# Optimization experiments

Measured on AMD Instinct MI355X. Metric: run time of the kernel, lower is better.

The kernel has to match this reference:

```python
import jax, jax.numpy as jnp
import numpy as np

TEMP = 0.07
LN_EPS = 1e-5


def _l2norm(x, eps=1e-12):
    n = jnp.linalg.norm(x, axis=-1, keepdims=True)
    return x / jnp.maximum(n, eps)


def setup_inputs() -> dict:
    key = jax.random.key(0)
    ks = jax.random.split(key, 8)
    B, N, D, S = 1024, 100000, 1024, 2
    scale = 1.0 / np.sqrt(D)
    return {
        "q": jax.random.normal(ks[0], (B, D), jnp.float32),
        "bank_values": jax.random.normal(ks[1], (N, D), jnp.float32),
        "proj_w": jax.random.normal(ks[2], (S, D, D), jnp.float32) * scale,
        "proj_b": jax.random.normal(ks[3], (S, D), jnp.float32) * 0.01,
        "unify_w": jax.random.normal(ks[4], (S, D, D), jnp.float32) * scale,
        "unify_b": jax.random.normal(ks[5], (S, D), jnp.float32) * 0.01,
        "ln_gamma": jnp.ones((D,), jnp.float32),
        "ln_beta": jnp.zeros((D,), jnp.float32),
        "top_m": 32,
    }


def reference(q, bank_values, proj_w, proj_b, unify_w, unify_b, ln_gamma, ln_beta, top_m):
    # PrototypeBank.build: keys = L2-normalized values (detached)
    keys = _l2norm(bank_values)  # [N, D]
    num_scales = proj_w.shape[0]
    ref = jnp.zeros_like(q)
    for s in range(num_scales):  # small fixed structural loop
        p = q @ proj_w[s].T + proj_b[s]                       # [B, D] Linear
        scores = _l2norm(p) @ keys.T                          # [B, N] cosine
        top_s, top_i = jax.lax.top_k(scores, top_m)           # [B, m]
        attn = jax.nn.softmax(top_s / TEMP, axis=-1)          # [B, m]
        z = jnp.einsum('bm,bmd->bd', attn, bank_values[top_i])  # weighted gather-sum
        ref = ref + z @ unify_w[s].T + unify_b[s]
    mu = ref.mean(axis=-1, keepdims=True)
    var = ref.var(axis=-1, keepdims=True)
    out = (ref - mu) * jax.lax.rsqrt(var + LN_EPS) * ln_gamma + ln_beta
    return out
```

## Files before the change

### kernel.cpp

```cpp
#include <hip/hip_runtime.h>
#include <math.h>


static inline size_t align256(size_t x){ return (x + 255) & ~size_t(255); }

typedef short bf16x8 __attribute__((ext_vector_type(8)));
typedef float f32x4  __attribute__((ext_vector_type(4)));

#define GLOAD_LDS16(gp, lp) \
  __builtin_amdgcn_global_load_lds((const __attribute__((address_space(1))) unsigned int*)(gp), \
                                   (__attribute__((address_space(3))) unsigned int*)(lp), 16, 0, 0)

__device__ inline unsigned short f2bf(float f){
  unsigned int u = __float_as_uint(f);
  u += 0x7fffu + ((u >> 16) & 1u);
  return (unsigned short)(u >> 16);
}
__device__ inline float bf2f(unsigned int h16){
  return __uint_as_float(h16 << 16);
}

template<bool SCALE_OUT>
__global__ __launch_bounds__(256) void rnorm_convert_kernel(
    const float* __restrict__ X, float* __restrict__ rn,
    unsigned short* __restrict__ out, int rows, int D)
{
  int wv = threadIdx.x >> 6, lane = threadIdx.x & 63;
  int r = blockIdx.x * 4 + wv;
  if (r >= rows) return;
  const float4* xr = (const float4*)(X + (size_t)r * D);
  int nv = D >> 2;
  float ss = 0.f;
  for (int i = lane; i < nv; i += 64){
    float4 v = xr[i];
    ss = fmaf(v.x,v.x, fmaf(v.y,v.y, fmaf(v.z,v.z, fmaf(v.w,v.w, ss))));
  }
  #pragma unroll
  for (int off = 32; off; off >>= 1) ss += __shfl_xor(ss, off);
  float rinv = 1.f / fmaxf(sqrtf(ss), 1e-12f);
  if (lane == 0) rn[r] = rinv;
  const float sc = SCALE_OUT ? rinv : 1.f;
  unsigned short* orow = out + (size_t)r * D;
  for (int i = lane; i < (D >> 3); i += 64){
    float4 v0 = xr[i*2], v1 = xr[i*2+1];
    v0.x*=sc; v0.y*=sc; v0.z*=sc; v0.w*=sc;
    v1.x*=sc; v1.y*=sc; v1.z*=sc; v1.w*=sc;
    uint4 w;
    w.x = (unsigned)f2bf(v0.x) | ((unsigned)f2bf(v0.y) << 16);
    w.y = (unsigned)f2bf(v0.z) | ((unsigned)f2bf(v0.w) << 16);
    w.z = (unsigned)f2bf(v1.x) | ((unsigned)f2bf(v1.y) << 16);
    w.w = (unsigned)f2bf(v1.z) | ((unsigned)f2bf(v1.w) << 16);
    *(uint4*)(orow + i*8) = w;
  }
}

template<int RM, int RN, bool ACCUM>
__global__ __launch_bounds__(256) void gemm_nt_kernel(
    const float* __restrict__ A, const float* __restrict__ B,
    const float* __restrict__ bias, const float* __restrict__ bscale,
    float* __restrict__ C, int M, int Nn, int K, int Brows, int ldc)
{
  __shared__ float As[16][RM*64 + 4];
  __shared__ float Bs[16][RN*64 + 4];
  const int t  = threadIdx.x;
  const int tm = t >> 4, tn = t & 15;
  const int m0 = blockIdx.y * (RM*64), n0 = blockIdx.x * (RN*64);

  float acc[RM][RN][4][4];
  #pragma unroll
  for (int r=0;r<RM;++r)
    #pragma unroll
    for (int c=0;c<RN;++c)
      #pragma unroll
      for (int i=0;i<4;++i)
        #pragma unroll
        for (int j=0;j<4;++j) acc[r][c][i][j]=0.f;

  for (int kp = 0; kp < K; kp += 16){
    #pragma unroll
    for (int l = 0; l < RM; ++l){
      int li = t + l*256;
      int row = li >> 2, kq = (li & 3) << 2;
      float4 v = *(const float4*)(A + (size_t)(m0+row)*K + kp + kq);
      As[kq+0][row]=v.x; As[kq+1][row]=v.y; As[kq+2][row]=v.z; As[kq+3][row]=v.w;
    }
    #pragma unroll
    for (int l = 0; l < RN; ++l){
      int li = t + l*256;
      int row = li >> 2, kq = (li & 3) << 2;
      int gn = n0 + row;
      float4 v = make_float4(0.f,0.f,0.f,0.f);
      float sc = 1.f;
      if (gn < Brows){
        v = *(const float4*)(B + (size_t)gn*K + kp + kq);
        if (bscale) sc = bscale[gn];
      }
      Bs[kq+0][row]=v.x*sc; Bs[kq+1][row]=v.y*sc; Bs[kq+2][row]=v.z*sc; Bs[kq+3][row]=v.w*sc;
    }
    __syncthreads();
    #pragma unroll
    for (int kk = 0; kk < 16; ++kk){
      float av[RM][4], bv[RN][4];
      #pragma unroll
      for (int r=0;r<RM;++r){
        float4 a = *(const float4*)&As[kk][r*64 + tm*4];
        av[r][0]=a.x; av[r][1]=a.y; av[r][2]=a.z; av[r][3]=a.w;
      }
      #pragma unroll
      for (int c=0;c<RN;++c){
        float4 b = *(const float4*)&Bs[kk][c*64 + tn*4];
        bv[c][0]=b.x; bv[c][1]=b.y; bv[c][2]=b.z; bv[c][3]=b.w;
      }
      #pragma unroll
      for (int r=0;r<RM;++r)
        #pragma unroll
        for (int c=0;c<RN;++c)
          #pragma unroll
          for (int i=0;i<4;++i)
            #pragma unroll
            for (int j=0;j<4;++j)
              acc[r][c][i][j] = fmaf(av[r][i], bv[c][j], acc[r][c][i][j]);
    }
    __syncthreads();
  }

  #pragma unroll
  for (int r=0;r<RM;++r){
    #pragma unroll
    for (int i=0;i<4;++i){
      int gm = m0 + r*64 + tm*4 + i;
      #pragma unroll
      for (int c=0;c<RN;++c){
        int gn = n0 + c*64 + tn*4;
        if (gn >= Nn) continue;
        float* cp = C + (size_t)gm*ldc + gn;
        float o0=acc[r][c][i][0], o1=acc[r][c][i][1], o2=acc[r][c][i][2], o3=acc[r][c][i][3];
        if (gn + 3 < Nn){
          float4 o = make_float4(o0,o1,o2,o3);
          if (bias){ float4 bb = *(const float4*)&bias[gn]; o.x+=bb.x; o.y+=bb.y; o.z+=bb.z; o.w+=bb.w; }
          if (ACCUM){ float4 cc = *(const float4*)cp; o.x+=cc.x; o.y+=cc.y; o.z+=cc.z; o.w+=cc.w; }
          *(float4*)cp = o;
        } else {
          float ov[4] = {o0,o1,o2,o3};
          for (int j=0;j<4;++j){
            if (gn + j < Nn){
              float o = ov[j];
              if (bias)  o += bias[gn+j];
              if (ACCUM) o += cp[j];
              cp[j] = o;
            }
          }
        }
      }
    }
  }
}

__global__ __launch_bounds__(256) void scores_mfma_kernel(
    const unsigned short* __restrict__ Abf, const unsigned short* __restrict__ Bbf,
    unsigned short* __restrict__ C, int M, int Nn, int K, int ldc)
{
  __shared__ __align__(16) unsigned char smem[32768];

  const int t = threadIdx.x;
  const int lane = t & 63, wid = t >> 6;
  const int wm = wid >> 1, wn = wid & 1;
  const int l15 = lane & 15, l4 = lane >> 4;

  const int nwg = gridDim.x;
  const int q = nwg >> 3, r = nwg & 7;
  const int xcd = blockIdx.x & 7, idx = blockIdx.x >> 3;
  const int logical = (xcd < r ? xcd*(q+1) : r*(q+1) + (xcd-r)*q) + idx;
  const int mtiles = M >> 7;
  const int m0 = (logical % mtiles) * 128;
  const int n0 = (logical / mtiles) * 128;

  f32x4 acc[4][4];
  #pragma unroll
  for (int i=0;i<4;++i)
    #pragma unroll
    for (int j=0;j<4;++j) acc[i][j] = (f32x4)0.f;

  const int srow = t >> 3;
  const int sb   = (t & 7) * 16;
  const int ldsb = wid * 1024;

  for (int kp = 0; kp < K; kp += 64){
    #pragma unroll
    for (int i = 0; i < 4; ++i){
      int row = srow + i*32;
      int src = sb ^ ((row & 7) << 4);
      const unsigned char* ga = (const unsigned char*)Abf
          + ((size_t)(m0+row)*K + kp)*2 + src;
      GLOAD_LDS16(ga, smem + i*4096 + ldsb);
      int gn = n0 + row; if (gn >= Nn) gn = Nn - 1;
      const unsigned char* gb = (const unsigned char*)Bbf
          + ((size_t)gn*K + kp)*2 + src;
      GLOAD_LDS16(gb, smem + 16384 + i*4096 + ldsb);
    }
    __syncthreads();

    const unsigned char* As_ = smem;
    const unsigned char* Bs_ = smem + 16384;
    bf16x8 B0[4], B1[4];
    #pragma unroll
    for (int fn = 0; fn < 4; ++fn){
      int br = wn*64 + fn*16 + l15;
      int xr = (br & 7) << 4;
      const unsigned char* bp = Bs_ + br*128;
      B0[fn] = *(const bf16x8*)(bp + (( l4*16      ) ^ xr));
      B1[fn] = *(const bf16x8*)(bp + ((64 + l4*16 ) ^ xr));
    }
    #pragma unroll
    for (int fm = 0; fm < 4; ++fm){
      int ar = wm*64 + fm*16 + l15;
      int xr = (ar & 7) << 4;
      const unsigned char* ap = As_ + ar*128;
      bf16x8 A0 = *(const bf16x8*)(ap + (( l4*16      ) ^ xr));
      bf16x8 A1 = *(const bf16x8*)(ap + ((64 + l4*16 ) ^ xr));
      #pragma unroll
      for (int fn = 0; fn < 4; ++fn){
        acc[fm][fn] = __builtin_amdgcn_mfma_f32_16x16x32_bf16(A0, B0[fn], acc[fm][fn], 0,0,0);
        acc[fm][fn] = __builtin_amdgcn_mfma_f32_16x16x32_bf16(A1, B1[fn], acc[fm][fn], 0,0,0);
      }
    }
    __syncthreads();
  }

  #pragma unroll
  for (int fm = 0; fm < 4; ++fm){
    int row = m0 + wm*64 + fm*16 + l4*4;
    #pragma unroll
    for (int fn = 0; fn < 4; ++fn){
      int col = n0 + wn*64 + fn*16 + l15;
      if (col < Nn){
        unsigned short* cp = C + (size_t)row*ldc + col;
        #pragma unroll
        for (int r2 = 0; r2 < 4; ++r2) cp[(size_t)r2*ldc] = f2bf(acc[fm][fn][r2]);
      }
    }
  }
}

__global__ __launch_bounds__(256) void chunk_filter_kernel(
    const unsigned short* __restrict__ scores, int ldc, int colbase, int Nwindow,
    int NC, float* __restrict__ cand_s, int* __restrict__ cand_i,
    int chunk0, int nchunks_total, int cap, float eps)
{
  extern __shared__ float lds[];
  __shared__ float sv[256];
  __shared__ float tau_s;
  __shared__ int cnt;
  const int row = blockIdx.x, t = threadIdx.x;
  const int lc = blockIdx.y;
  const int col0l = lc * NC;
  int ncols = Nwindow - col0l; if (ncols > NC) ncols = NC;
  const int gchunk = chunk0 + lc;
  const unsigned short* sr = scores + (size_t)row * ldc + col0l;

  float m0 = -INFINITY, m1 = -INFINITY, m2 = -INFINITY, m3 = -INFINITY;
  const int nc8 = ncols >> 3;
  const uint4* sr8 = (const uint4*)sr;
  float4* lds4 = (float4*)lds;
  for (int j = t; j < nc8; j += 256){
    uint4 v = sr8[j];
    float4 a = make_float4(bf2f(v.x & 0xffffu), bf2f(v.x >> 16),
                           bf2f(v.y & 0xffffu), bf2f(v.y >> 16));
    float4 b = make_float4(bf2f(v.z & 0xffffu), bf2f(v.z >> 16),
                           bf2f(v.w & 0xffffu), bf2f(v.w >> 16));
    lds4[j*2]   = a;
    lds4[j*2+1] = b;
    m0 = fmaxf(m0, fmaxf(a.x, b.x)); m1 = fmaxf(m1, fmaxf(a.y, b.y));
    m2 = fmaxf(m2, fmaxf(a.z, b.z)); m3 = fmaxf(m3, fmaxf(a.w, b.w));
  }
  for (int j = (nc8 << 3) + t; j < ncols; j += 256){
    float v = bf2f((unsigned)sr[j]);
    lds[j] = v;
    m0 = fmaxf(m0, v);
  }
  sv[t] = fmaxf(fmaxf(m0, m1), fmaxf(m2, m3));
  __syncthreads();

  for (int k = 2; k <= 256; k <<= 1){
    for (int j = k >> 1; j > 0; j >>= 1){
      int p = t ^ j;
      float a = sv[t], b = sv[p];
      bool up = ((t & k) == 0);
      float keep = (t < p) ? (up ? fmaxf(a,b) : fminf(a,b))
                           : (up ? fminf(a,b) : fmaxf(a,b));
      __syncthreads();
      sv[t] = keep;
      __syncthreads();
    }
  }
  if (t == 0){ tau_s = sv[31]; cnt = 0; }
  __syncthreads();
  const float thr = tau_s - eps;

  float* cs = cand_s + ((size_t)row * nchunks_total + gchunk) * cap;
  int*   ci = cand_i + ((size_t)row * nchunks_total + gchunk) * cap;

  for (int j = t; j < ncols; j += 256){
    float v = lds[j];
    if (v >= thr){
      int pos = atomicAdd(&cnt, 1);
      if (pos < cap){ cs[pos] = v; ci[pos] = colbase + col0l + j; }
    }
  }
  __syncthreads();
  int n = cnt < cap ? cnt : cap;
  for (int j = n + t; j < cap; j += 256) ci[j] = -1;
}

__global__ __launch_bounds__(256) void select_softmax_gather_kernel(
    const float* __restrict__ cand_s, const int* __restrict__ cand_i,
    const float* __restrict__ p, const float* __restrict__ rn_bank,
    const float* __restrict__ pnorm, const float* __restrict__ bank,
    float* __restrict__ z, int ncap, int D, int topm, float invtemp, float eps)
{
  __shared__ float p_s[1024];
  __shared__ float vs[1024]; __shared__ int vi[1024];
  __shared__ float sv[256];
  __shared__ int   cidx[256];
  __shared__ float rv[256];
  __shared__ float tau_s;
  __shared__ int cnt;
  const int row = blockIdx.x, t = threadIdx.x;
  const int lane = t & 63, wid = t >> 6;

  const float4* pr = (const float4*)(p + (size_t)row * D);
  for (int i = t; i < (D >> 2); i += 256) ((float4*)p_s)[i] = pr[i];
  const float* cs = cand_s + (size_t)row * ncap;
  const int*  ci = cand_i + (size_t)row * ncap;
  for (int j = t; j < ncap; j += 256){
    int k = ci[j];
    vi[j] = k;
    vs[j] = (k >= 0) ? cs[j] : -INFINITY;
  }
  __syncthreads();

  float m = -INFINITY;
  for (int j = t; j < ncap; j += 256) m = fmaxf(m, vs[j]);
  sv[t] = m;
  __syncthreads();
  for (int k = 2; k <= 256; k <<= 1){
    for (int j = k >> 1; j > 0; j >>= 1){
      int pp = t ^ j;
      float a = sv[t], b = sv[pp];
      bool up = ((t & k) == 0);
      float keep = (t < pp) ? (up ? fmaxf(a,b) : fminf(a,b))
                            : (up ? fminf(a,b) : fmaxf(a,b));
      __syncthreads();
      sv[t] = keep;
      __syncthreads();
    }
  }
  if (t == 0){ tau_s = sv[31]; cnt = 0; }
  __syncthreads();
  const float thr = tau_s - eps;

  for (int j = t; j < ncap; j += 256){
    if (vi[j] >= 0 && vs[j] >= thr){
      int pos = atomicAdd(&cnt, 1);
      if (pos < 256) cidx[pos] = vi[j];
    }
  }
  __syncthreads();
  const int n2 = cnt < 256 ? cnt : 256;
  rv[t] = -INFINITY;
  if (t >= n2) cidx[t] = 0x7fffffff;
  __syncthreads();

  const int nj = D >> 8;
  for (int c = wid; c < n2; c += 4){
    int idx = cidx[c];
    const float4* kr = (const float4*)(bank + (size_t)idx * D);
    float ss = 0.f;
    for (int j = 0; j < nj; ++j){
      float4 kv = kr[lane + j*64];
      float4 pv = *(const float4*)&p_s[(lane + j*64) << 2];
      ss = fmaf(pv.x,kv.x, fmaf(pv.y,kv.y, fmaf(pv.z,kv.z, fmaf(pv.w,kv.w, ss))));
    }
    #pragma unroll
    for (int off = 32; off; off >>= 1) ss += __shfl_xor(ss, off);
    if (lane == 0) rv[c] = ss * rn_bank[idx];
  }
  __syncthreads();

  for (int k = 2; k <= 256; k <<= 1){
    for (int j = k >> 1; j > 0; j >>= 1){
      int pp = t ^ j;
      float av = rv[t];  int ai = cidx[t];
      float bv = rv[pp]; int bi = cidx[pp];
      bool up = ((t & k) == 0);
      bool agtb = (av > bv) || (av == bv && ai < bi);
      bool keepA = (t < pp) ? (up ? agtb : !agtb)
                            : (up ? !agtb : agtb);
      __syncthreads();
      if (keepA){ rv[t] = av; cidx[t] = ai; } else { rv[t] = bv; cidx[t] = bi; }
      __syncthreads();
    }
  }

  if (t == 0){
    float pn = pnorm[row] * invtemp;
    float mx = rv[0] * pn;
    float sum = 0.f;
    for (int i = 0; i < topm; ++i){
      float w = expf(rv[i]*pn - mx);
      sv[i] = w; sum += w;
    }
    float inv = 1.f / sum;
    for (int i = 0; i < topm; ++i) sv[i] *= inv;
  }
  __syncthreads();

  for (int d4 = t; d4 < (D >> 2); d4 += 256){
    float ax=0.f, ay=0.f, az=0.f, aw=0.f;
    for (int i = 0; i < topm; ++i){
      float a = sv[i];
      const float4 v = *(const float4*)(bank + (size_t)cidx[i]*D + (d4<<2));
      ax = fmaf(a, v.x, ax); ay = fmaf(a, v.y, ay);
      az = fmaf(a, v.z, az); aw = fmaf(a, v.w, aw);
    }
    *(float4*)(z + (size_t)row*D + (d4<<2)) = make_float4(ax,ay,az,aw);
  }
}

__global__ __launch_bounds__(256) void layernorm_kernel(
    const float* __restrict__ ref, const float* __restrict__ gamma,
    const float* __restrict__ beta, float* __restrict__ out, int D, float eps)
{
  __shared__ float s1[4], s2[4];
  const int row = blockIdx.x, t = threadIdx.x;
  const float4* xr = (const float4*)(ref + (size_t)row*D);
  int nv = D >> 2;
  float sum = 0.f, ssq = 0.f;
  for (int i = t; i < nv; i += 256){
    float4 v = xr[i];
    sum += v.x+v.y+v.z+v.w;
    ssq = fmaf(v.x,v.x, fmaf(v.y,v.y, fmaf(v.z,v.z, fmaf(v.w,v.w, ssq))));
  }
  const int lane = t & 63, wid = t >> 6;
  #pragma unroll
  for (int off = 32; off; off >>= 1){ sum += __shfl_xor(sum, off); ssq += __shfl_xor(ssq, off); }
  if (lane == 0){ s1[wid] = sum; s2[wid] = ssq; }
  __syncthreads();
  sum = s1[0]+s1[1]+s1[2]+s1[3];
  ssq = s2[0]+s2[1]+s2[2]+s2[3];
  float mu  = sum / (float)D;
  float var = ssq / (float)D - mu*mu;
  float rs  = rsqrtf(var + eps);
  const float4* g4 = (const float4*)gamma;
  const float4* b4 = (const float4*)beta;
  float4* o4 = (float4*)(out + (size_t)row*D);
  for (int i = t; i < nv; i += 256){
    float4 v = xr[i], g = g4[i], bb = b4[i];
    float4 o;
    o.x = (v.x-mu)*rs*g.x + bb.x;
    o.y = (v.y-mu)*rs*g.y + bb.y;
    o.z = (v.z-mu)*rs*g.z + bb.z;
    o.w = (v.w-mu)*rs*g.w + bb.w;
    o4[i] = o;
  }
}

extern "C" void kernel_launch(void* const* d_in, const int* in_sizes, int n_in,
                              void* d_out, int out_size, void* d_ws, size_t ws_size,
                              hipStream_t stream)
{
  const float* q       = (const float*)d_in[0];
  const float* bank    = (const float*)d_in[1];
  const float* proj_w  = (const float*)d_in[2];
  const float* proj_b  = (const float*)d_in[3];
  const float* unify_w = (const float*)d_in[4];
  const float* unify_b = (const float*)d_in[5];
  const float* gamma   = (const float*)d_in[6];
  const float* beta    = (const float*)d_in[7];

  const int D = in_sizes[6];
  const int B = in_sizes[0] / D;
  const int N = in_sizes[1] / D;
  const int S = in_sizes[2] / (D * D);
  const int R = S * B;
  const int TOPM = 32;
  const int CAP  = 64;
  const int NC   = 12544;
  const float INVTEMP = 1.0f / 0.07f;
  const float EPS = 0.025f;

  const int NCH = (N + NC - 1) / NC;

  char* wsb = (char*)d_ws;
  size_t off = 0;
  auto take = [&](size_t bytes)->char*{ char* p = wsb + off; off += align256(bytes); return p; };
  float* rn_bank = (float*)take((size_t)N*4);
  float* pnorm   = (float*)take((size_t)R*4);
  float* p       = (float*)take((size_t)R*D*4);
  float* z       = (float*)take((size_t)R*D*4);
  float* ref     = (float*)take((size_t)B*D*4);
  float* cand_s  = (float*)take((size_t)R*NCH*CAP*4);
  int*   cand_i  = (int*)  take((size_t)R*NCH*CAP*4);
  unsigned short* bank_bf = (unsigned short*)take((size_t)N*D*2);
  unsigned short* p_bf    = (unsigned short*)take((size_t)R*D*2);
  unsigned short* scores  = (unsigned short*)take((size_t)R*(size_t)N*2);

  rnorm_convert_kernel<true><<<(N+3)/4, 256, 0, stream>>>(
      bank, rn_bank, bank_bf, N, D);

  dim3 g1(D/64, B/64);
  for (int s = 0; s < S; ++s)
    gemm_nt_kernel<1,1,false><<<g1, 256, 0, stream>>>(
        q, proj_w + (size_t)s*D*D, proj_b + (size_t)s*D, nullptr,
        p + (size_t)s*B*D, B, D, D, D, D);

  rnorm_convert_kernel<false><<<(R+3)/4, 256, 0, stream>>>(
      p, pnorm, p_bf, R, D);

  {
    int ntile = (N + 127) / 128;
    int nwg = (R / 128) * ntile;
    scores_mfma_kernel<<<nwg, 256, 0, stream>>>(
        p_bf, bank_bf, scores, R, N, D, N);
    chunk_filter_kernel<<<dim3(R, NCH), 256, (size_t)NC*4, stream>>>(
        scores, N, 0, N, NC, cand_s, cand_i,
        0, NCH, CAP, EPS);
  }

  select_softmax_gather_kernel<<<R, 256, 0, stream>>>(
      cand_s, cand_i, p, rn_bank, pnorm, bank, z,
      NCH*CAP, D, TOPM, INVTEMP, EPS);

  for (int s = 0; s < S; ++s){
    if (s == 0)
      gemm_nt_kernel<1,1,false><<<g1, 256, 0, stream>>>(
          z + (size_t)s*B*D, unify_w + (size_t)s*D*D, unify_b + (size_t)s*D, nullptr,
          ref, B, D, D, D, D);
    else
      gemm_nt_kernel<1,1,true><<<g1, 256, 0, stream>>>(
          z + (size_t)s*B*D, unify_w + (size_t)s*D*D, unify_b + (size_t)s*D, nullptr,
          ref, B, D, D, D, D);
  }

  layernorm_kernel<<<B, 256, 0, stream>>>(ref, gamma, beta, (float*)d_out, D, 1e-5f);
}
```

Baseline: 1.398 ms.

## Fuse per-scale unify GEMMs into one K-concatenated GEMM and simplify scores grid

Writes the gathered z vectors for both scales into one concatenated [B, S*D] buffer and packs the unify weights into a matching [D, S*D] layout. The two unify GEMMs (the second with read-modify-write accumulation) then become a single GEMM with K=2048 and two bias adds. This removes one kernel launch and the extra read/write of ref, at the cost of an added weight-packing pass every call. Separately, the XCD-aware block remapping in the scores MFMA kernel is replaced with a plain 2D grid, which may change L2 locality on the largest kernel.

```diff
diff --git a/kernel.cpp b/kernel.cpp
--- a/kernel.cpp
+++ b/kernel.cpp
@@ -54,10 +54,27 @@
   }
 }
 
+__global__ __launch_bounds__(256) void pack_wcat_kernel(
+    const float* __restrict__ W, float* __restrict__ wcat, int D, int S)
+{
+  long total4 = (long)D * S * D / 4;
+  long i = (long)blockIdx.x * 256 + threadIdx.x;
+  const long stride = (long)gridDim.x * 256;
+  const int SD = S * D;
+  for (; i < total4; i += stride){
+    long e = i * 4;
+    int n = (int)(e / SD);
+    int c = (int)(e % SD);
+    int s = c / D, k = c % D;
+    float4 v = *(const float4*)(W + (size_t)s*D*D + (size_t)n*D + k);
+    *(float4*)(wcat + e) = v;
+  }
+}
+
 template<int RM, int RN, bool ACCUM>
 __global__ __launch_bounds__(256) void gemm_nt_kernel(
     const float* __restrict__ A, const float* __restrict__ B,
-    const float* __restrict__ bias, const float* __restrict__ bscale,
+    const float* __restrict__ bias, const float* __restrict__ bias2,
     float* __restrict__ C, int M, int Nn, int K, int Brows, int ldc)
 {
   __shared__ float As[16][RM*64 + 4];
@@ -90,12 +107,9 @@
       int row = li >> 2, kq = (li & 3) << 2;
       int gn = n0 + row;
       float4 v = make_float4(0.f,0.f,0.f,0.f);
-      float sc = 1.f;
-      if (gn < Brows){
+      if (gn < Brows)
         v = *(const float4*)(B + (size_t)gn*K + kp + kq);
-        if (bscale) sc = bscale[gn];
-      }
-      Bs[kq+0][row]=v.x*sc; Bs[kq+1][row]=v.y*sc; Bs[kq+2][row]=v.z*sc; Bs[kq+3][row]=v.w*sc;
+      Bs[kq+0][row]=v.x; Bs[kq+1][row]=v.y; Bs[kq+2][row]=v.z; Bs[kq+3][row]=v.w;
     }
     __syncthreads();
     #pragma unroll
@@ -138,6 +152,7 @@
         if (gn + 3 < Nn){
           float4 o = make_float4(o0,o1,o2,o3);
           if (bias){ float4 bb = *(const float4*)&bias[gn]; o.x+=bb.x; o.y+=bb.y; o.z+=bb.z; o.w+=bb.w; }
+          if (bias2){ float4 bb = *(const float4*)&bias2[gn]; o.x+=bb.x; o.y+=bb.y; o.z+=bb.z; o.w+=bb.w; }
           if (ACCUM){ float4 cc = *(const float4*)cp; o.x+=cc.x; o.y+=cc.y; o.z+=cc.z; o.w+=cc.w; }
           *(float4*)cp = o;
         } else {
@@ -146,6 +161,7 @@
             if (gn + j < Nn){
               float o = ov[j];
               if (bias)  o += bias[gn+j];
+              if (bias2) o += bias2[gn+j];
               if (ACCUM) o += cp[j];
               cp[j] = o;
             }
@@ -166,14 +182,7 @@
   const int lane = t & 63, wid = t >> 6;
   const int wm = wid >> 1, wn = wid & 1;
   const int l15 = lane & 15, l4 = lane >> 4;
-
-  const int nwg = gridDim.x;
-  const int q = nwg >> 3, r = nwg & 7;
-  const int xcd = blockIdx.x & 7, idx = blockIdx.x >> 3;
-  const int logical = (xcd < r ? xcd*(q+1) : r*(q+1) + (xcd-r)*q) + idx;
-  const int mtiles = M >> 7;
-  const int m0 = (logical % mtiles) * 128;
-  const int n0 = (logical / mtiles) * 128;
+  const int m0 = blockIdx.x * 128, n0 = blockIdx.y * 128;
 
   f32x4 acc[4][4];
   #pragma unroll
@@ -316,7 +325,8 @@
     const float* __restrict__ cand_s, const int* __restrict__ cand_i,
     const float* __restrict__ p, const float* __restrict__ rn_bank,
     const float* __restrict__ pnorm, const float* __restrict__ bank,
-    float* __restrict__ z, int ncap, int D, int topm, float invtemp, float eps)
+    float* __restrict__ zcat, int srows, int ncap, int D, int topm,
+    float invtemp, float eps)
 {
   __shared__ float p_s[1024];
   __shared__ float vs[1024]; __shared__ int vi[1024];
@@ -415,6 +425,10 @@
   }
   __syncthreads();
 
+  const int s = row / srows, b = row % srows;
+  float* zr = zcat + (size_t)b * (2ull * D) * 0 ;
+  const int S = gridDim.x / srows;
+  zr = zcat + (size_t)b * ((size_t)S * D) + (size_t)s * D;
   for (int d4 = t; d4 < (D >> 2); d4 += 256){
     float ax=0.f, ay=0.f, az=0.f, aw=0.f;
     for (int i = 0; i < topm; ++i){
@@ -423,7 +437,7 @@
       ax = fmaf(a, v.x, ax); ay = fmaf(a, v.y, ay);
       az = fmaf(a, v.z, az); aw = fmaf(a, v.w, aw);
     }
-    *(float4*)(z + (size_t)row*D + (d4<<2)) = make_float4(ax,ay,az,aw);
+    *(float4*)(zr + (d4<<2)) = make_float4(ax,ay,az,aw);
   }
 }
 
@@ -483,6 +497,7 @@
   const int N = in_sizes[1] / D;
   const int S = in_sizes[2] / (D * D);
   const int R = S * B;
+  const int SD = S * D;
   const int TOPM = 32;
   const int CAP  = 64;
   const int NC   = 12544;
@@ -497,7 +512,8 @@
   float* rn_bank = (float*)take((size_t)N*4);
   float* pnorm   = (float*)take((size_t)R*4);
   float* p       = (float*)take((size_t)R*D*4);
-  float* z       = (float*)take((size_t)R*D*4);
+  float* zcat    = (float*)take((size_t)B*SD*4);
+  float* wcat    = (float*)take((size_t)D*SD*4);
   float* ref     = (float*)take((size_t)B*D*4);
   float* cand_s  = (float*)take((size_t)R*NCH*CAP*4);
   int*   cand_i  = (int*)  take((size_t)R*NCH*CAP*4);
@@ -507,6 +523,7 @@
 
   rnorm_convert_kernel<true><<<(N+3)/4, 256, 0, stream>>>(
       bank, rn_bank, bank_bf, N, D);
+  pack_wcat_kernel<<<512, 256, 0, stream>>>(unify_w, wcat, D, S);
 
   dim3 g1(D/64, B/64);
   for (int s = 0; s < S; ++s)
@@ -518,9 +535,8 @@
       p, pnorm, p_bf, R, D);
 
   {
-    int ntile = (N + 127) / 128;
-    int nwg = (R / 128) * ntile;
-    scores_mfma_kernel<<<nwg, 256, 0, stream>>>(
+    dim3 g2(R/128, (N + 127)/128);
+    scores_mfma_kernel<<<g2, 256, 0, stream>>>(
         p_bf, bank_bf, scores, R, N, D, N);
     chunk_filter_kernel<<<dim3(R, NCH), 256, (size_t)NC*4, stream>>>(
         scores, N, 0, N, NC, cand_s, cand_i,
@@ -528,19 +544,12 @@
   }
 
   select_softmax_gather_kernel<<<R, 256, 0, stream>>>(
-      cand_s, cand_i, p, rn_bank, pnorm, bank, z,
+      cand_s, cand_i, p, rn_bank, pnorm, bank, zcat, B,
       NCH*CAP, D, TOPM, INVTEMP, EPS);
 
-  for (int s = 0; s < S; ++s){
-    if (s == 0)
-      gemm_nt_kernel<1,1,false><<<g1, 256, 0, stream>>>(
-          z + (size_t)s*B*D, unify_w + (size_t)s*D*D, unify_b + (size_t)s*D, nullptr,
-          ref, B, D, D, D, D);
-    else
-      gemm_nt_kernel<1,1,true><<<g1, 256, 0, stream>>>(
-          z + (size_t)s*B*D, unify_w + (size_t)s*D*D, unify_b + (size_t)s*D, nullptr,
-          ref, B, D, D, D, D);
-  }
+  gemm_nt_kernel<1,1,false><<<g1, 256, 0, stream>>>(
+      zcat, wcat, unify_b, unify_b + D,
+      ref, B, D, SD, D, D);
 
   layernorm_kernel<<<B, 256, 0, stream>>>(ref, gamma, beta, (float*)d_out, D, 1e-5f);
 }
```

New measurement: 1.385 ms. Within noise of the previous version (-0.9%).
